# Kernel tuning notes

Measured on AMD Instinct MI355X. Metric: run time of the kernel, lower is better.

Reference implementation:

```python
import jax, jax.numpy as jnp
import numpy as np

EPS = 1e-4

def _softmax_features(x, proj, is_query):
    # x: [B,H,N,D], proj: [M,D] -> features [B,H,N,M] (FAVOR+ softmax kernel)
    d = x.shape[-1]
    m = proj.shape[0]
    data_normalizer = d ** -0.25
    ratio = m ** -0.5
    xd = jnp.einsum('bhnd,md->bhnm', x * data_normalizer, proj)
    diag = 0.5 * (data_normalizer ** 2) * jnp.sum(x * x, axis=-1, keepdims=True)  # [B,H,N,1]
    if is_query:
        mx = jax.lax.stop_gradient(jnp.max(xd, axis=-1, keepdims=True))
    else:
        mx = jax.lax.stop_gradient(jnp.max(xd, axis=(-1, -2), keepdims=True))
    return ratio * (jnp.exp(xd - diag - mx) + EPS)

def setup_inputs() -> dict:
    key = jax.random.key(0)
    kq, kk, kv, kp = jax.random.split(key, 4)
    B, H, N, D, M = 4, 8, 8192, 64, 256
    Q = jax.random.normal(kq, (B, H, N, D), dtype=jnp.float32)
    K = jax.random.normal(kk, (B, H, N, D), dtype=jnp.float32)
    V = jax.random.normal(kv, (B, H, N, D), dtype=jnp.float32)
    mask = jnp.ones((B, N), dtype=jnp.float32)
    proj = jax.random.normal(kp, (M, D), dtype=jnp.float32)
    return {'Q': Q, 'K': K, 'V': V, 'mask': mask, 'proj': proj}

def reference(Q, K, V, mask, proj):
    # Mask keys/values before the kernel, as in the torch module
    Km = K * mask[:, None, :, None]
    Vm = V * mask[:, None, :, None]
    q = _softmax_features(Q, proj, is_query=True)    # [B,H,N,M]
    k = _softmax_features(Km, proj, is_query=False)  # [B,H,N,M]
    # Non-causal linear attention: out = q (k^T v) / (q k_sum)
    k_sum = jnp.sum(k, axis=-2)                         # [B,H,M]
    d_inv = 1.0 / jnp.einsum('bhnm,bhm->bhn', q, k_sum)  # [B,H,N]
    ctx = jnp.einsum('bhnm,bhnd->bhmd', k, Vm)            # [B,H,M,D]
    out = jnp.einsum('bhnm,bhmd,bhn->bhnd', q, ctx, d_inv)
    return out
```

## Files before the change

### kernel.cpp

```cpp
#include <hip/hip_runtime.h>


typedef __attribute__((ext_vector_type(8))) short short8;
typedef __attribute__((ext_vector_type(8))) _Float16 half8;
typedef __attribute__((ext_vector_type(4))) float f32x4;

namespace {
constexpr int BN = 8192, DD = 64, MM = 256, NHEADS = 32;
constexpr float CNORM = 0.35355339059327373f;
constexpr float FEPS  = 1e-4f;
constexpr float INV2048 = 4.8828125e-4f;

constexpr size_t OFF_BX    = 0;
constexpr size_t OFF_CS    = 8192;
constexpr size_t OFF_KSUMP = 270336;
constexpr size_t OFF_KSUMG = 335872;
constexpr size_t OFF_VSP   = 344320;
constexpr size_t OFF_CTXP  = 360704;
}

__device__ __forceinline__ unsigned short f2bf(float f) {
  unsigned u = __float_as_uint(f);
  u += 0x7fffu + ((u >> 16) & 1u);
  return (unsigned short)(u >> 16);
}
__device__ __forceinline__ float bf2f(unsigned short h) {
  return __uint_as_float(((unsigned)h) << 16);
}
__device__ __forceinline__ unsigned pk2(unsigned short a, unsigned short b) {
  return (unsigned)a | ((unsigned)b << 16);
}
__device__ __forceinline__ unsigned short f2h(float f) {
  _Float16 h = (_Float16)f;
  return __builtin_bit_cast(unsigned short, h);
}
__device__ __forceinline__ float h2f(unsigned short u) {
  return (float)__builtin_bit_cast(_Float16, u);
}

template <int T>
__device__ __forceinline__ void xcd_map(int& bh, int& tile) {
  int id = blockIdx.y * T + blockIdx.x;
  int xcd = id & 7, s = id >> 3;
  bh = xcd * 4 + s / T;
  tile = s % T;
}

__global__ void kPrep(const float* __restrict__ proj, unsigned short* __restrict__ BxG) {
  int s = blockIdx.x * 256 + threadIdx.x;
  int l = s & 63, kb = (s >> 6) & 1, mt = s >> 7;
  int n = mt * 16 + (l & 15);
  int k0 = kb * 32 + (l >> 4) * 8;
  unsigned short o[8];
#pragma unroll
  for (int j = 0; j < 8; ++j) o[j] = f2h(proj[n * 64 + k0 + j]);
  *(uint4*)(BxG + (size_t)s * 8) =
      make_uint4(pk2(o[0], o[1]), pk2(o[2], o[3]), pk2(o[4], o[5]), pk2(o[6], o[7]));
}

__global__ void __launch_bounds__(512, 4)
kCtx(const float* __restrict__ Kin, const float* __restrict__ Vin,
     const float* __restrict__ mask, const unsigned short* __restrict__ BxG,
     float* __restrict__ ctxp, float* __restrict__ ksump,
     float* __restrict__ mxg, float* __restrict__ vsp) {
  __shared__ __align__(16) unsigned short BxH[8192];
  __shared__ __align__(16) unsigned short Fs[128 * 140];
  __shared__ __align__(16) unsigned short VF[16 * 64 * 8];
  __shared__ float wmax[8];
  __shared__ float ksred[1024];
  __shared__ float vred[512];
  const int tid = threadIdx.x;
  int bh, tl16;
  xcd_map<16>(bh, tl16);
  const int tile = tl16 >> 1, mh = tl16 & 1;
  const int b = bh >> 3;
  const float* Kh = Kin + (size_t)bh * BN * DD;
  const float* Vh = Vin + (size_t)bh * BN * DD;
  const float* mrow = mask + (size_t)b * BN;
#pragma unroll
  for (int i = 0; i < 2; ++i)
    ((uint4*)BxH)[tid + i * 512] = ((const uint4*)BxG)[mh * 1024 + tid + i * 512];
  const int w = tid >> 6, l = tid & 63, lm = l & 15, kl = l >> 4;
  const int lmv = tid & 15, klnv = (tid >> 4) & 3, dtv = (tid >> 6) & 3, ksv0 = tid >> 8;

  f32x4 cacc[4];
#pragma unroll
  for (int dt = 0; dt < 4; ++dt) cacc[dt] = f32x4{0.f, 0.f, 0.f, 0.f};
  float kspart[8] = {0.f, 0.f, 0.f, 0.f, 0.f, 0.f, 0.f, 0.f};
  float wm = -3e38f, vsum = 0.f;

  const int rbase = tile * 1024;
  float4 kv0, kv1, kv2, kv3;
  float mskK;
  {
    const float* rp = Kh + (size_t)(rbase + w * 16 + lm) * 64 + kl * 8;
    kv0 = *(const float4*)rp;        kv1 = *(const float4*)(rp + 4);
    kv2 = *(const float4*)(rp + 32); kv3 = *(const float4*)(rp + 36);
    mskK = mrow[rbase + w * 16 + lm];
  }
  __syncthreads();

  for (int ch = 0; ch < 8; ++ch) {
    const int r0 = rbase + ch * 128;
    half8 ah0, ah1, al0, al1;
    float diagv;
    {
      float scale = CNORM * mskK;
      float x[16] = {kv0.x, kv0.y, kv0.z, kv0.w, kv1.x, kv1.y, kv1.z, kv1.w,
                     kv2.x, kv2.y, kv2.z, kv2.w, kv3.x, kv3.y, kv3.z, kv3.w};
      float sq = 0.f;
#pragma unroll
      for (int e = 0; e < 16; ++e) {
        float y = x[e] * scale;
        _Float16 h = (_Float16)y;
        _Float16 lo = (_Float16)((y - (float)h) * 2048.0f);
        if (e < 8) { ah0[e] = h; al0[e] = lo; } else { ah1[e - 8] = h; al1[e - 8] = lo; }
        sq = fmaf(y, y, sq);
      }
      sq += __shfl_xor(sq, 16);
      sq += __shfl_xor(sq, 32);
      diagv = 0.5f * sq;
    }
    {
      const int nr = rbase + ((ch + 1) & 7) * 128 + w * 16 + lm;
      const float* rp = Kh + (size_t)nr * 64 + kl * 8;
      kv0 = *(const float4*)rp;        kv1 = *(const float4*)(rp + 4);
      kv2 = *(const float4*)(rp + 32); kv3 = *(const float4*)(rp + 36);
      mskK = mrow[nr];
    }
    float vv[16];
#pragma unroll
    for (int h = 0; h < 2; ++h) {
      int nb = (ksv0 * 2 + h) * 32 + klnv * 8;
#pragma unroll
      for (int j = 0; j < 8; ++j)
        vv[h * 8 + j] = Vh[(size_t)(r0 + nb + j) * 64 + dtv * 16 + lmv];
    }
    float dgv[4];
#pragma unroll
    for (int r = 0; r < 4; ++r)
      dgv[r] = __shfl(diagv, (l & 48) + kl * 4 + r);
#pragma unroll
    for (int j = 0; j < 8; ++j) {
      half8 b0 = *(const half8*)&BxH[((j * 2 + 0) * 64 + l) * 8];
      half8 b1 = *(const half8*)&BxH[((j * 2 + 1) * 64 + l) * 8];
      f32x4 a0 = {0.f, 0.f, 0.f, 0.f}, a1 = {0.f, 0.f, 0.f, 0.f};
      a0 = __builtin_amdgcn_mfma_f32_16x16x32_f16(ah0, b0, a0, 0, 0, 0);
      a0 = __builtin_amdgcn_mfma_f32_16x16x32_f16(ah1, b1, a0, 0, 0, 0);
      a1 = __builtin_amdgcn_mfma_f32_16x16x32_f16(al0, b0, a1, 0, 0, 0);
      a1 = __builtin_amdgcn_mfma_f32_16x16x32_f16(al1, b1, a1, 0, 0, 0);
      float x0 = fmaf(a1[0], INV2048, a0[0]);
      float x1 = fmaf(a1[1], INV2048, a0[1]);
      float x2 = fmaf(a1[2], INV2048, a0[2]);
      float x3 = fmaf(a1[3], INV2048, a0[3]);
      wm = fmaxf(wm, fmaxf(fmaxf(x0, x1), fmaxf(x2, x3)));
      float f0 = __expf(x0 - dgv[0]);
      float f1 = __expf(x1 - dgv[1]);
      float f2 = __expf(x2 - dgv[2]);
      float f3 = __expf(x3 - dgv[3]);
      kspart[j] += f0 + f1 + f2 + f3;
      *(uint2*)&Fs[(j * 16 + lm) * 140 + w * 16 + kl * 4] =
          make_uint2(pk2(f2bf(f0), f2bf(f1)), pk2(f2bf(f2), f2bf(f3)));
    }
#pragma unroll
    for (int h = 0; h < 2; ++h) {
      int ks = ksv0 * 2 + h;
      int nb = ks * 32 + klnv * 8;
      float4 m0 = *(const float4*)&mrow[r0 + nb];
      float4 m1 = *(const float4*)&mrow[r0 + nb + 4];
      float mk[8] = {m0.x, m0.y, m0.z, m0.w, m1.x, m1.y, m1.z, m1.w};
      unsigned short o[8];
#pragma unroll
      for (int j = 0; j < 8; ++j) {
        float vmv = vv[h * 8 + j] * mk[j];
        o[j] = f2bf(vmv);
        vsum += vmv;
      }
      *(uint4*)&VF[((ks * 4 + dtv) * 64 + klnv * 16 + lmv) * 8] =
          make_uint4(pk2(o[0], o[1]), pk2(o[2], o[3]), pk2(o[4], o[5]), pk2(o[6], o[7]));
    }
    __syncthreads();
#pragma unroll
    for (int ks = 0; ks < 4; ++ks) {
      union { short8 v; uint2 u[2]; } af;
      const int ab = (w * 16 + lm) * 140 + ks * 32 + kl * 8;
      af.u[0] = *(const uint2*)&Fs[ab];
      af.u[1] = *(const uint2*)&Fs[ab + 4];
#pragma unroll
      for (int dt = 0; dt < 4; ++dt) {
        short8 vb = *(const short8*)&VF[((ks * 4 + dt) * 64 + l) * 8];
        cacc[dt] = __builtin_amdgcn_mfma_f32_16x16x32_bf16(af.v, vb, cacc[dt], 0, 0, 0);
      }
    }
    __syncthreads();
  }
#pragma unroll
  for (int j = 0; j < 8; ++j) {
    kspart[j] += __shfl_xor(kspart[j], 16);
    kspart[j] += __shfl_xor(kspart[j], 32);
  }
  if (l < 16) {
#pragma unroll
    for (int j = 0; j < 8; ++j) ksred[(j * 16 + l) * 8 + w] = kspart[j];
  }
  {
    wm = fmaxf(wm, __shfl_xor(wm, 1));  wm = fmaxf(wm, __shfl_xor(wm, 2));
    wm = fmaxf(wm, __shfl_xor(wm, 4));  wm = fmaxf(wm, __shfl_xor(wm, 8));
    wm = fmaxf(wm, __shfl_xor(wm, 16)); wm = fmaxf(wm, __shfl_xor(wm, 32));
    if (l == 0) wmax[w] = wm;
  }
  vred[tid] = vsum;
  __syncthreads();
  if (tid < 128) {
    float s = 0.f;
#pragma unroll
    for (int k = 0; k < 8; ++k) s += ksred[tid * 8 + k];
    ksump[(size_t)(bh * 16 + tl16) * 128 + tid] = s;
  }
  if (mh == 0 && tid < 64) {
    float vs = 0.f;
#pragma unroll
    for (int k = 0; k < 8; ++k)
      vs += vred[(k >> 2) * 256 + (tid >> 4) * 64 + (k & 3) * 16 + (tid & 15)];
    vsp[(size_t)(bh * 8 + tile) * 64 + tid] = vs;
  }
  if (tid == 0) {
    float bm = wmax[0];
#pragma unroll
    for (int i = 1; i < 8; ++i) bm = fmaxf(bm, wmax[i]);
    mxg[bh * 256 + 240 + tl16] = bm;
  }
  float* cp = ctxp + (size_t)(bh * 16 + tl16) * 8192;
#pragma unroll
  for (int dt = 0; dt < 4; ++dt)
#pragma unroll
    for (int r = 0; r < 4; ++r)
      cp[(w * 16 + kl * 4 + r) * 64 + dt * 16 + lm] = cacc[dt][r];
}

__global__ void kRedCtx(const float* __restrict__ ctxp, const float* __restrict__ ksump,
                        const float* __restrict__ vsp, unsigned short* __restrict__ CsG,
                        float* __restrict__ ksumG) {
  __shared__ __align__(16) float ctxL[16384];
  __shared__ float vsL[64];
  const int bh = blockIdx.x, t = threadIdx.x;
  float MX = -3e38f;
#pragma unroll
  for (int i = 0; i < 16; ++i) MX = fmaxf(MX, ksumG[bh * 256 + 240 + i]);
  const float fsc = __expf(-MX);
  __syncthreads();
#pragma unroll
  for (int i = 0; i < 16; ++i) {
    int idx4 = t + i * 256;
    int mhi = (idx4 >> 11) & 1;
    int loc = idx4 & 2047;
    float4 s = make_float4(0.f, 0.f, 0.f, 0.f);
#pragma unroll
    for (int tl = 0; tl < 8; ++tl) {
      float4 a = ((const float4*)(ctxp + (size_t)(bh * 16 + tl * 2 + mhi) * 8192))[loc];
      s.x += a.x; s.y += a.y; s.z += a.z; s.w += a.w;
    }
    s.x *= fsc; s.y *= fsc; s.z *= fsc; s.w *= fsc;
    ((float4*)ctxL)[idx4] = s;
  }
  {
    int mhi = t >> 7, loc = t & 127;
    float ks = 0.f;
#pragma unroll
    for (int tl = 0; tl < 8; ++tl)
      ks += ksump[(size_t)(bh * 16 + tl * 2 + mhi) * 128 + loc];
    ksumG[bh * 256 + t] = fsc * ks + FEPS * (float)BN;
  }
  if (t < 64) {
    float vs = 0.f;
#pragma unroll
    for (int tl = 0; tl < 8; ++tl) vs += vsp[(size_t)(bh * 8 + tl) * 64 + t];
    vsL[t] = vs;
  }
  __syncthreads();
#pragma unroll
  for (int i = 0; i < 8; ++i) {
    int slot = t + i * 256;
    int l = slot & 63, s = (slot >> 6) & 7, dt = slot >> 9;
    int d = dt * 16 + (l & 15);
    int mb = s * 32 + (l >> 4) * 8;
    float ve = FEPS * vsL[d];
    unsigned short o[8];
#pragma unroll
    for (int j = 0; j < 8; ++j) o[j] = f2bf(ctxL[(mb + j) * 64 + d] + ve);
    *(uint4*)(CsG + (size_t)bh * 16384 + (size_t)slot * 8) =
        make_uint4(pk2(o[0], o[1]), pk2(o[2], o[3]), pk2(o[4], o[5]), pk2(o[6], o[7]));
  }
}

__global__ void __launch_bounds__(512, 1)
kOut(const float* __restrict__ Qin, const unsigned short* __restrict__ BxG,
     const unsigned short* __restrict__ CsG, const float* __restrict__ ksumG,
     float* __restrict__ outp) {
  __shared__ __align__(16) unsigned short BxH[16384];
  __shared__ __align__(16) unsigned short Ff[128 * 264];
  __shared__ float den[128];
  const int tid = threadIdx.x;
  int bh, tile;
  xcd_map<8>(bh, tile);
  const float* Qh = Qin + (size_t)bh * BN * DD;
  const unsigned short* CsB = CsG + (size_t)bh * 16384;
  const int w = tid >> 6, l = tid & 63, lm = l & 15, kl = l >> 4;
#pragma unroll
  for (int i = 0; i < 4; ++i)
    ((uint4*)BxH)[tid + i * 512] = ((const uint4*)BxG)[tid + i * 512];
  short8 cb[8];
#pragma unroll
  for (int s = 0; s < 8; ++s)
    cb[s] = *(const short8*)(CsB + (size_t)((((w >> 1) * 8 + s) * 64 + l) * 8));
  float kss[16];
#pragma unroll
  for (int j = 0; j < 16; ++j) kss[j] = ksumG[bh * 256 + j * 16 + lm];
  __syncthreads();

  for (int ch = 0; ch < 8; ++ch) {
    const int r0 = tile * 1024 + ch * 128;
    const size_t rowoff = (size_t)(r0 + w * 16 + lm) * 64;
    float4 v0 = *(const float4*)(Qh + rowoff + kl * 8);
    float4 v1 = *(const float4*)(Qh + rowoff + kl * 8 + 4);
    float4 v2 = *(const float4*)(Qh + rowoff + 32 + kl * 8);
    float4 v3 = *(const float4*)(Qh + rowoff + 32 + kl * 8 + 4);
    half8 ah0, ah1, al0, al1;
    float sq = 0.f;
    {
      float x[16] = {v0.x, v0.y, v0.z, v0.w, v1.x, v1.y, v1.z, v1.w,
                     v2.x, v2.y, v2.z, v2.w, v3.x, v3.y, v3.z, v3.w};
#pragma unroll
      for (int e = 0; e < 16; ++e) {
        float y = x[e] * CNORM;
        _Float16 h = (_Float16)y;
        _Float16 lo = (_Float16)((y - (float)h) * 2048.0f);
        if (e < 8) { ah0[e] = h; al0[e] = lo; } else { ah1[e - 8] = h; al1[e - 8] = lo; }
        sq = fmaf(y, y, sq);
      }
      sq += __shfl_xor(sq, 16);
      sq += __shfl_xor(sq, 32);
    }
    const float diagv = 0.5f * sq;
    f32x4 accC[16];
#pragma unroll
    for (int j = 0; j < 16; ++j) {
      half8 b0 = *(const half8*)&BxH[((j * 2 + 0) * 64 + l) * 8];
      half8 b1 = *(const half8*)&BxH[((j * 2 + 1) * 64 + l) * 8];
      f32x4 acc0 = {0.f, 0.f, 0.f, 0.f}, acc1 = {0.f, 0.f, 0.f, 0.f};
      acc0 = __builtin_amdgcn_mfma_f32_16x16x32_f16(ah0, b0, acc0, 0, 0, 0);
      acc0 = __builtin_amdgcn_mfma_f32_16x16x32_f16(ah1, b1, acc0, 0, 0, 0);
      acc1 = __builtin_amdgcn_mfma_f32_16x16x32_f16(al0, b0, acc1, 0, 0, 0);
      acc1 = __builtin_amdgcn_mfma_f32_16x16x32_f16(al1, b1, acc1, 0, 0, 0);
#pragma unroll
      for (int r = 0; r < 4; ++r) accC[j][r] = fmaf(acc1[r], INV2048, acc0[r]);
    }
    float mrow[4];
#pragma unroll
    for (int r = 0; r < 4; ++r) {
      float m0 = accC[0][r];
#pragma unroll
      for (int j = 1; j < 16; ++j) m0 = fmaxf(m0, accC[j][r]);
      m0 = fmaxf(m0, __shfl_xor(m0, 1));
      m0 = fmaxf(m0, __shfl_xor(m0, 2));
      m0 = fmaxf(m0, __shfl_xor(m0, 4));
      m0 = fmaxf(m0, __shfl_xor(m0, 8));
      mrow[r] = m0;
    }
    float dgv[4], dnn[4] = {0.f, 0.f, 0.f, 0.f};
#pragma unroll
    for (int r = 0; r < 4; ++r)
      dgv[r] = __shfl(diagv, (l & 48) + kl * 4 + r) + mrow[r];
#pragma unroll
    for (int j = 0; j < 16; ++j) {
#pragma unroll
      for (int r = 0; r < 4; ++r) {
        float q = __expf(accC[j][r] - dgv[r]) + FEPS;
        unsigned short qh = f2bf(q);
        Ff[(w * 16 + kl * 4 + r) * 264 + j * 16 + lm] = qh;
        dnn[r] += bf2f(qh) * kss[j];
      }
    }
#pragma unroll
    for (int r = 0; r < 4; ++r) {
      dnn[r] += __shfl_xor(dnn[r], 1); dnn[r] += __shfl_xor(dnn[r], 2);
      dnn[r] += __shfl_xor(dnn[r], 4); dnn[r] += __shfl_xor(dnn[r], 8);
    }
    if (lm == 0) {
#pragma unroll
      for (int r = 0; r < 4; ++r) den[w * 16 + kl * 4 + r] = 1.0f / dnn[r];
    }
    __syncthreads();
    const int prow = (w & 1) * 64, pd = (w >> 1) * 16;
    f32x4 oacc[4];
#pragma unroll
    for (int fr = 0; fr < 4; ++fr) oacc[fr] = f32x4{0.f, 0.f, 0.f, 0.f};
#pragma unroll
    for (int s = 0; s < 8; ++s) {
#pragma unroll
      for (int fr = 0; fr < 4; ++fr) {
        short8 af = *(const short8*)&Ff[(prow + fr * 16 + lm) * 264 + s * 32 + kl * 8];
        oacc[fr] = __builtin_amdgcn_mfma_f32_16x16x32_bf16(af, cb[s], oacc[fr], 0, 0, 0);
      }
    }
#pragma unroll
    for (int fr = 0; fr < 4; ++fr) {
#pragma unroll
      for (int r = 0; r < 4; ++r) {
        int n = prow + fr * 16 + kl * 4 + r;
        outp[((size_t)bh * BN + r0 + n) * 64 + pd + lm] = oacc[fr][r] * den[n];
      }
    }
    __syncthreads();
  }
}

extern "C" void kernel_launch(void* const* d_in, const int* in_sizes, int n_in,
                              void* d_out, int out_size, void* d_ws, size_t ws_size,
                              hipStream_t stream) {
  const float* Q    = (const float*)d_in[0];
  const float* K    = (const float*)d_in[1];
  const float* V    = (const float*)d_in[2];
  const float* mask = (const float*)d_in[3];
  const float* proj = (const float*)d_in[4];
  float* out = (float*)d_out;
  float* ws = (float*)d_ws;

  unsigned short* wBx = (unsigned short*)(ws + OFF_BX);
  unsigned short* wCs = (unsigned short*)(ws + OFF_CS);
  float* wKsump = ws + OFF_KSUMP;
  float* wKsumG = ws + OFF_KSUMG;
  float* wVsp   = ws + OFF_VSP;
  float* wCtxp  = ws + OFF_CTXP;

  kPrep<<<8, 256, 0, stream>>>(proj, wBx);
  kCtx<<<dim3(16, NHEADS), 512, 0, stream>>>(K, V, mask, wBx, wCtxp, wKsump, wKsumG, wVsp);
  kRedCtx<<<NHEADS, 256, 0, stream>>>(wCtxp, wKsump, wVsp, wCs, wKsumG);
  kOut<<<dim3(8, NHEADS), 512, 0, stream>>>(Q, wBx, wCs, wKsumG, out);
}
```

Baseline: 141.3 us.

## Restructure output kernel to keep query features in registers and fuse denominator

The output kernel now computes the feature projection transposed, so each lane holds one row's features. It rebuilds the MFMA A-operand with lane shuffles instead of staging features through LDS with a block barrier. The denominator is computed by an extra MFMA against a hi/lo bf16 split of k_sum that the reduction kernel writes into a reused workspace slot. The context matrix now lives in LDS rather than registers, the grid is doubled with 512-row tiles, and the next Q chunk is prefetched. Separately, both feature kernels fold log2(e) into the scaling so they can call hardware v_exp_f32 directly, and they use packed v_cvt_pk_bf16_f32 conversions; this trades a little precision and adds register pressure from the per-lane feature arrays.

After: 216.0 us. 1.53x slower.

```diff
diff --git a/kernel.cpp b/kernel.cpp
--- a/kernel.cpp
+++ b/kernel.cpp
@@ -8,6 +8,8 @@
 namespace {
 constexpr int BN = 8192, DD = 64, MM = 256, NHEADS = 32;
 constexpr float CNORM = 0.35355339059327373f;
+constexpr float LOG2E = 1.4426950408889634f;
+constexpr float DGC   = 0.34657359027997264f;
 constexpr float FEPS  = 1e-4f;
 constexpr float INV2048 = 4.8828125e-4f;
 
@@ -34,8 +36,15 @@
   _Float16 h = (_Float16)f;
   return __builtin_bit_cast(unsigned short, h);
 }
-__device__ __forceinline__ float h2f(unsigned short u) {
-  return (float)__builtin_bit_cast(_Float16, u);
+__device__ __forceinline__ float exp2hw(float x) {
+  float r;
+  asm("v_exp_f32 %0, %1" : "=v"(r) : "v"(x));
+  return r;
+}
+__device__ __forceinline__ unsigned cvtpk(float lo, float hi) {
+  unsigned r;
+  asm("v_cvt_pk_bf16_f32 %0, %1, %2" : "=v"(r) : "v"(lo), "v"(hi));
+  return r;
 }
 
 template <int T>
@@ -105,7 +114,7 @@
     half8 ah0, ah1, al0, al1;
     float diagv;
     {
-      float scale = CNORM * mskK;
+      float scale = CNORM * LOG2E * mskK;
       float x[16] = {kv0.x, kv0.y, kv0.z, kv0.w, kv1.x, kv1.y, kv1.z, kv1.w,
                      kv2.x, kv2.y, kv2.z, kv2.w, kv3.x, kv3.y, kv3.z, kv3.w};
       float sq = 0.f;
@@ -119,7 +128,7 @@
       }
       sq += __shfl_xor(sq, 16);
       sq += __shfl_xor(sq, 32);
-      diagv = 0.5f * sq;
+      diagv = DGC * sq;
     }
     {
       const int nr = rbase + ((ch + 1) & 7) * 128 + w * 16 + lm;
@@ -154,13 +163,13 @@
       float x2 = fmaf(a1[2], INV2048, a0[2]);
       float x3 = fmaf(a1[3], INV2048, a0[3]);
       wm = fmaxf(wm, fmaxf(fmaxf(x0, x1), fmaxf(x2, x3)));
-      float f0 = __expf(x0 - dgv[0]);
-      float f1 = __expf(x1 - dgv[1]);
-      float f2 = __expf(x2 - dgv[2]);
-      float f3 = __expf(x3 - dgv[3]);
+      float f0 = exp2hw(x0 - dgv[0]);
+      float f1 = exp2hw(x1 - dgv[1]);
+      float f2 = exp2hw(x2 - dgv[2]);
+      float f3 = exp2hw(x3 - dgv[3]);
       kspart[j] += f0 + f1 + f2 + f3;
       *(uint2*)&Fs[(j * 16 + lm) * 140 + w * 16 + kl * 4] =
-          make_uint2(pk2(f2bf(f0), f2bf(f1)), pk2(f2bf(f2), f2bf(f3)));
+          make_uint2(cvtpk(f0, f1), cvtpk(f2, f3));
     }
 #pragma unroll
     for (int h = 0; h < 2; ++h) {
@@ -169,15 +178,15 @@
       float4 m0 = *(const float4*)&mrow[r0 + nb];
       float4 m1 = *(const float4*)&mrow[r0 + nb + 4];
       float mk[8] = {m0.x, m0.y, m0.z, m0.w, m1.x, m1.y, m1.z, m1.w};
-      unsigned short o[8];
+      float vm[8];
 #pragma unroll
       for (int j = 0; j < 8; ++j) {
-        float vmv = vv[h * 8 + j] * mk[j];
-        o[j] = f2bf(vmv);
-        vsum += vmv;
+        vm[j] = vv[h * 8 + j] * mk[j];
+        vsum += vm[j];
       }
       *(uint4*)&VF[((ks * 4 + dtv) * 64 + klnv * 16 + lmv) * 8] =
-          make_uint4(pk2(o[0], o[1]), pk2(o[2], o[3]), pk2(o[4], o[5]), pk2(o[6], o[7]));
+          make_uint4(cvtpk(vm[0], vm[1]), cvtpk(vm[2], vm[3]),
+                     cvtpk(vm[4], vm[5]), cvtpk(vm[6], vm[7]));
     }
     __syncthreads();
 #pragma unroll
@@ -240,14 +249,14 @@
 
 __global__ void kRedCtx(const float* __restrict__ ctxp, const float* __restrict__ ksump,
                         const float* __restrict__ vsp, unsigned short* __restrict__ CsG,
-                        float* __restrict__ ksumG) {
+                        float* __restrict__ ksumG, unsigned short* __restrict__ wKf) {
   __shared__ __align__(16) float ctxL[16384];
   __shared__ float vsL[64];
   const int bh = blockIdx.x, t = threadIdx.x;
   float MX = -3e38f;
 #pragma unroll
   for (int i = 0; i < 16; ++i) MX = fmaxf(MX, ksumG[bh * 256 + 240 + i]);
-  const float fsc = __expf(-MX);
+  const float fsc = exp2hw(-MX);
   __syncthreads();
 #pragma unroll
   for (int i = 0; i < 16; ++i) {
@@ -263,13 +272,15 @@
     s.x *= fsc; s.y *= fsc; s.z *= fsc; s.w *= fsc;
     ((float4*)ctxL)[idx4] = s;
   }
+  float ks2;
   {
     int mhi = t >> 7, loc = t & 127;
     float ks = 0.f;
 #pragma unroll
     for (int tl = 0; tl < 8; ++tl)
       ks += ksump[(size_t)(bh * 16 + tl * 2 + mhi) * 128 + loc];
-    ksumG[bh * 256 + t] = fsc * ks + FEPS * (float)BN;
+    ks2 = fsc * ks + FEPS * (float)BN;
+    ksumG[bh * 256 + t] = ks2;
   }
   if (t < 64) {
     float vs = 0.f;
@@ -278,6 +289,14 @@
     vsL[t] = vs;
   }
   __syncthreads();
+  {
+    unsigned short khi = f2bf(ks2);
+    unsigned short klo = f2bf(ks2 - bf2f(khi));
+    unsigned short* kfb = wKf + (size_t)bh * 1024;
+    int idx = (t >> 3) * 16 + (t & 7);
+    kfb[idx] = khi;
+    kfb[idx + 8] = klo;
+  }
 #pragma unroll
   for (int i = 0; i < 8; ++i) {
     int slot = t + i * 256;
@@ -293,125 +312,134 @@
   }
 }
 
-__global__ void __launch_bounds__(512, 1)
+__global__ void __launch_bounds__(512, 4)
 kOut(const float* __restrict__ Qin, const unsigned short* __restrict__ BxG,
-     const unsigned short* __restrict__ CsG, const float* __restrict__ ksumG,
+     const unsigned short* __restrict__ CsG, const unsigned short* __restrict__ KfG,
      float* __restrict__ outp) {
   __shared__ __align__(16) unsigned short BxH[16384];
-  __shared__ __align__(16) unsigned short Ff[128 * 264];
-  __shared__ float den[128];
+  __shared__ __align__(16) unsigned short CsL[16384];
+  __shared__ __align__(16) unsigned short KfL[528];
   const int tid = threadIdx.x;
   int bh, tile;
-  xcd_map<8>(bh, tile);
+  xcd_map<16>(bh, tile);
   const float* Qh = Qin + (size_t)bh * BN * DD;
-  const unsigned short* CsB = CsG + (size_t)bh * 16384;
   const int w = tid >> 6, l = tid & 63, lm = l & 15, kl = l >> 4;
 #pragma unroll
   for (int i = 0; i < 4; ++i)
     ((uint4*)BxH)[tid + i * 512] = ((const uint4*)BxG)[tid + i * 512];
-  short8 cb[8];
-#pragma unroll
-  for (int s = 0; s < 8; ++s)
-    cb[s] = *(const short8*)(CsB + (size_t)((((w >> 1) * 8 + s) * 64 + l) * 8));
-  float kss[16];
-#pragma unroll
-  for (int j = 0; j < 16; ++j) kss[j] = ksumG[bh * 256 + j * 16 + lm];
+#pragma unroll
+  for (int i = 0; i < 4; ++i)
+    ((uint4*)CsL)[tid + i * 512] = ((const uint4*)(CsG + (size_t)bh * 16384))[tid + i * 512];
+  if (tid < 256) ((unsigned*)KfL)[tid] = ((const unsigned*)(KfG + (size_t)bh * 1024))[tid];
+  if (tid >= 256 && tid < 264) ((unsigned*)KfL)[tid] = 0u;
+  float4 kv0, kv1, kv2, kv3;
+  {
+    const float* rp = Qh + (size_t)(tile * 512 + w * 16 + lm) * 64 + kl * 8;
+    kv0 = *(const float4*)rp;        kv1 = *(const float4*)(rp + 4);
+    kv2 = *(const float4*)(rp + 32); kv3 = *(const float4*)(rp + 36);
+  }
   __syncthreads();
 
-  for (int ch = 0; ch < 8; ++ch) {
-    const int r0 = tile * 1024 + ch * 128;
-    const size_t rowoff = (size_t)(r0 + w * 16 + lm) * 64;
-    float4 v0 = *(const float4*)(Qh + rowoff + kl * 8);
-    float4 v1 = *(const float4*)(Qh + rowoff + kl * 8 + 4);
-    float4 v2 = *(const float4*)(Qh + rowoff + 32 + kl * 8);
-    float4 v3 = *(const float4*)(Qh + rowoff + 32 + kl * 8 + 4);
-    half8 ah0, ah1, al0, al1;
-    float sq = 0.f;
+  for (int ch = 0; ch < 4; ++ch) {
+    const int r0 = tile * 512 + ch * 128;
+    half8 bh0, bh1, bl0, bl1;
+    float diagv;
     {
-      float x[16] = {v0.x, v0.y, v0.z, v0.w, v1.x, v1.y, v1.z, v1.w,
-                     v2.x, v2.y, v2.z, v2.w, v3.x, v3.y, v3.z, v3.w};
+      const float scale = CNORM * LOG2E;
+      float x[16] = {kv0.x, kv0.y, kv0.z, kv0.w, kv1.x, kv1.y, kv1.z, kv1.w,
+                     kv2.x, kv2.y, kv2.z, kv2.w, kv3.x, kv3.y, kv3.z, kv3.w};
+      float sq = 0.f;
 #pragma unroll
       for (int e = 0; e < 16; ++e) {
-        float y = x[e] * CNORM;
+        float y = x[e] * scale;
         _Float16 h = (_Float16)y;
         _Float16 lo = (_Float16)((y - (float)h) * 2048.0f);
-        if (e < 8) { ah0[e] = h; al0[e] = lo; } else { ah1[e - 8] = h; al1[e - 8] = lo; }
+        if (e < 8) { bh0[e] = h; bl0[e] = lo; } else { bh1[e - 8] = h; bl1[e - 8] = lo; }
         sq = fmaf(y, y, sq);
       }
       sq += __shfl_xor(sq, 16);
       sq += __shfl_xor(sq, 32);
-    }
-    const float diagv = 0.5f * sq;
+      diagv = DGC * sq;
+    }
+    {
+      const int nr = tile * 512 + ((ch + 1) & 3) * 128 + w * 16 + lm;
+      const float* rp = Qh + (size_t)nr * 64 + kl * 8;
+      kv0 = *(const float4*)rp;        kv1 = *(const float4*)(rp + 4);
+      kv2 = *(const float4*)(rp + 32); kv3 = *(const float4*)(rp + 36);
+    }
     f32x4 accC[16];
 #pragma unroll
     for (int j = 0; j < 16; ++j) {
-      half8 b0 = *(const half8*)&BxH[((j * 2 + 0) * 64 + l) * 8];
-      half8 b1 = *(const half8*)&BxH[((j * 2 + 1) * 64 + l) * 8];
-      f32x4 acc0 = {0.f, 0.f, 0.f, 0.f}, acc1 = {0.f, 0.f, 0.f, 0.f};
-      acc0 = __builtin_amdgcn_mfma_f32_16x16x32_f16(ah0, b0, acc0, 0, 0, 0);
-      acc0 = __builtin_amdgcn_mfma_f32_16x16x32_f16(ah1, b1, acc0, 0, 0, 0);
-      acc1 = __builtin_amdgcn_mfma_f32_16x16x32_f16(al0, b0, acc1, 0, 0, 0);
-      acc1 = __builtin_amdgcn_mfma_f32_16x16x32_f16(al1, b1, acc1, 0, 0, 0);
-#pragma unroll
-      for (int r = 0; r < 4; ++r) accC[j][r] = fmaf(acc1[r], INV2048, acc0[r]);
-    }
-    float mrow[4];
+      half8 a0 = *(const half8*)&BxH[((j * 2 + 0) * 64 + l) * 8];
+      half8 a1 = *(const half8*)&BxH[((j * 2 + 1) * 64 + l) * 8];
+      f32x4 c0 = {0.f, 0.f, 0.f, 0.f}, c1 = {0.f, 0.f, 0.f, 0.f};
+      c0 = __builtin_amdgcn_mfma_f32_16x16x32_f16(a0, bh0, c0, 0, 0, 0);
+      c0 = __builtin_amdgcn_mfma_f32_16x16x32_f16(a1, bh1, c0, 0, 0, 0);
+      c1 = __builtin_amdgcn_mfma_f32_16x16x32_f16(a0, bl0, c1, 0, 0, 0);
+      c1 = __builtin_amdgcn_mfma_f32_16x16x32_f16(a1, bl1, c1, 0, 0, 0);
+#pragma unroll
+      for (int r = 0; r < 4; ++r) accC[j][r] = fmaf(c1[r], INV2048, c0[r]);
+    }
+    float mrow;
+    {
+      float m0 = accC[0][0];
+#pragma unroll
+      for (int j = 0; j < 16; ++j)
+#pragma unroll
+        for (int r = 0; r < 4; ++r) m0 = fmaxf(m0, accC[j][r]);
+      m0 = fmaxf(m0, __shfl_xor(m0, 16));
+      m0 = fmaxf(m0, __shfl_xor(m0, 32));
+      mrow = m0;
+    }
+    const float dgv = diagv + mrow;
+    unsigned pk[16][2];
+#pragma unroll
+    for (int j = 0; j < 16; ++j) {
+      float f0 = exp2hw(accC[j][0] - dgv) + FEPS;
+      float f1 = exp2hw(accC[j][1] - dgv) + FEPS;
+      float f2 = exp2hw(accC[j][2] - dgv) + FEPS;
+      float f3 = exp2hw(accC[j][3] - dgv) + FEPS;
+      pk[j][0] = cvtpk(f0, f1);
+      pk[j][1] = cvtpk(f2, f3);
+    }
+    f32x4 oacc[4], acc4;
+#pragma unroll
+    for (int dt = 0; dt < 4; ++dt) oacc[dt] = f32x4{0.f, 0.f, 0.f, 0.f};
+    acc4 = f32x4{0.f, 0.f, 0.f, 0.f};
+#pragma unroll
+    for (int ks = 0; ks < 8; ++ks) {
+      union { short8 v; unsigned u[4]; } af;
+#pragma unroll
+      for (int p = 0; p < 4; ++p) {
+        int sl = ((kl & 1) * 2 + (p >> 1)) * 16 + lm;
+        unsigned va = __shfl(pk[2 * ks][p & 1], sl);
+        unsigned vb = __shfl(pk[2 * ks + 1][p & 1], sl);
+        af.u[p] = (kl & 2) ? vb : va;
+      }
+#pragma unroll
+      for (int dt = 0; dt < 4; ++dt) {
+        short8 vb2 = *(const short8*)&CsL[((dt * 8 + ks) * 64 + l) * 8];
+        oacc[dt] = __builtin_amdgcn_mfma_f32_16x16x32_bf16(af.v, vb2, oacc[dt], 0, 0, 0);
+      }
+      int ko = (lm < 2) ? ((ks * 4 + kl) * 16 + lm * 8) : 512;
+      short8 kf = *(const short8*)&KfL[ko];
+      acc4 = __builtin_amdgcn_mfma_f32_16x16x32_bf16(af.v, kf, acc4, 0, 0, 0);
+    }
+    float dv[4];
 #pragma unroll
     for (int r = 0; r < 4; ++r) {
-      float m0 = accC[0][r];
-#pragma unroll
-      for (int j = 1; j < 16; ++j) m0 = fmaxf(m0, accC[j][r]);
-      m0 = fmaxf(m0, __shfl_xor(m0, 1));
-      m0 = fmaxf(m0, __shfl_xor(m0, 2));
-      m0 = fmaxf(m0, __shfl_xor(m0, 4));
-      m0 = fmaxf(m0, __shfl_xor(m0, 8));
-      mrow[r] = m0;
-    }
-    float dgv[4], dnn[4] = {0.f, 0.f, 0.f, 0.f};
-#pragma unroll
-    for (int r = 0; r < 4; ++r)
-      dgv[r] = __shfl(diagv, (l & 48) + kl * 4 + r) + mrow[r];
-#pragma unroll
-    for (int j = 0; j < 16; ++j) {
+      float t2 = acc4[r] + __shfl_xor(acc4[r], 1);
+      float rd = 1.0f / t2;
+      dv[r] = __shfl(rd, l & 48);
+    }
+#pragma unroll
+    for (int dt = 0; dt < 4; ++dt) {
 #pragma unroll
       for (int r = 0; r < 4; ++r) {
-        float q = __expf(accC[j][r] - dgv[r]) + FEPS;
-        unsigned short qh = f2bf(q);
-        Ff[(w * 16 + kl * 4 + r) * 264 + j * 16 + lm] = qh;
-        dnn[r] += bf2f(qh) * kss[j];
-      }
-    }
-#pragma unroll
-    for (int r = 0; r < 4; ++r) {
-      dnn[r] += __shfl_xor(dnn[r], 1); dnn[r] += __shfl_xor(dnn[r], 2);
-      dnn[r] += __shfl_xor(dnn[r], 4); dnn[r] += __shfl_xor(dnn[r], 8);
-    }
-    if (lm == 0) {
-#pragma unroll
-      for (int r = 0; r < 4; ++r) den[w * 16 + kl * 4 + r] = 1.0f / dnn[r];
-    }
-    __syncthreads();
-    const int prow = (w & 1) * 64, pd = (w >> 1) * 16;
-    f32x4 oacc[4];
-#pragma unroll
-    for (int fr = 0; fr < 4; ++fr) oacc[fr] = f32x4{0.f, 0.f, 0.f, 0.f};
-#pragma unroll
-    for (int s = 0; s < 8; ++s) {
-#pragma unroll
-      for (int fr = 0; fr < 4; ++fr) {
-        short8 af = *(const short8*)&Ff[(prow + fr * 16 + lm) * 264 + s * 32 + kl * 8];
-        oacc[fr] = __builtin_amdgcn_mfma_f32_16x16x32_bf16(af, cb[s], oacc[fr], 0, 0, 0);
-      }
-    }
-#pragma unroll
-    for (int fr = 0; fr < 4; ++fr) {
-#pragma unroll
-      for (int r = 0; r < 4; ++r) {
-        int n = prow + fr * 16 + kl * 4 + r;
-        outp[((size_t)bh * BN + r0 + n) * 64 + pd + lm] = oacc[fr][r] * den[n];
-      }
-    }
-    __syncthreads();
+        outp[((size_t)bh * BN + r0 + w * 16 + kl * 4 + r) * 64 + dt * 16 + lm] =
+            oacc[dt][r] * dv[r];
+      }
+    }
   }
 }
 
@@ -431,10 +459,11 @@
   float* wKsump = ws + OFF_KSUMP;
   float* wKsumG = ws + OFF_KSUMG;
   float* wVsp   = ws + OFF_VSP;
+  unsigned short* wKf = (unsigned short*)(ws + OFF_VSP);
   float* wCtxp  = ws + OFF_CTXP;
 
   kPrep<<<8, 256, 0, stream>>>(proj, wBx);
   kCtx<<<dim3(16, NHEADS), 512, 0, stream>>>(K, V, mask, wBx, wCtxp, wKsump, wKsumG, wVsp);
-  kRedCtx<<<NHEADS, 256, 0, stream>>>(wCtxp, wKsump, wVsp, wCs, wKsumG);
-  kOut<<<dim3(8, NHEADS), 512, 0, stream>>>(Q, wBx, wCs, wKsumG, out);
-}
+  kRedCtx<<<NHEADS, 256, 0, stream>>>(wCtxp, wKsump, wVsp, wCs, wKsumG, wKf);
+  kOut<<<dim3(16, NHEADS), 512, 0, stream>>>(Q, wBx, wCs, wKf, out);
+}
```
